# Performance work log

Measured on AMD Instinct MI355X. Metric: run time of the kernel, lower is better.

The kernel has to match this reference:

```python
import jax, jax.numpy as jnp
import numpy as np

B, T, C = 2, 1024, 2048
NH, NKV = 16, 4
HD = C // NH          # 128
NUM_REP = NH // NKV   # 4


def _apply_rotation(x, angles):
    # x: (B, T, nh, hd); angles: (T, hd//2). Equivalent to the per-pair 2x2
    # rotation matmuls in the torch code: [x0', x1'] = [[cos,-sin],[sin,cos]] @ [x0, x1]
    Bx, Tx, nh, hd = x.shape
    xp = x.reshape(Bx, Tx, nh, hd // 2, 2)
    cos = jnp.cos(angles)[None, :, None, :]  # (1, T, 1, hd//2)
    sin = jnp.sin(angles)[None, :, None, :]
    x0, x1 = xp[..., 0], xp[..., 1]
    rot = jnp.stack([cos * x0 - sin * x1, sin * x0 + cos * x1], axis=-1)
    return rot.reshape(Bx, Tx, nh, hd)


def setup_inputs() -> dict:
    key = jax.random.key(0)
    ks = jax.random.split(key, 5)
    x = jax.random.normal(ks[0], (B, T, C), dtype=jnp.float32)
    # standard RoPE angle table: pos * 10000^(-2i/hd), shape (T, hd//2)
    inv_freq = 1.0 / (10000.0 ** (jnp.arange(0, HD, 2, dtype=jnp.float32) / HD))
    angles = jnp.arange(T, dtype=jnp.float32)[:, None] * inv_freq[None, :]
    s = 0.02
    wq = jax.random.normal(ks[1], (C, C), dtype=jnp.float32) * s
    wk = jax.random.normal(ks[2], (C, NKV * HD), dtype=jnp.float32) * s
    wv = jax.random.normal(ks[3], (C, NKV * HD), dtype=jnp.float32) * s
    wo = jax.random.normal(ks[4], (C, C), dtype=jnp.float32) * s
    return {"x": x, "angles": angles, "wq": wq, "wk": wk, "wv": wv, "wo": wo}


def reference(x, angles, wq, wk, wv, wo):
    Bx, Tx, Cx = x.shape
    q = (x @ wq).reshape(Bx, Tx, NH, HD)
    k = (x @ wk).reshape(Bx, Tx, NKV, HD)
    v = (x @ wv).reshape(Bx, Tx, NKV, HD)
    q = _apply_rotation(q, angles)
    k = _apply_rotation(k, angles)
    q = q.transpose(0, 2, 1, 3)  # (B, nh, T, hd)
    k = k.transpose(0, 2, 1, 3)  # (B, nkv, T, hd)
    v = v.transpose(0, 2, 1, 3)
    if NKV != 1:
        # torch .repeat tiles kv heads: query head h uses kv head h % NKV
        k = jnp.tile(k, (1, NUM_REP, 1, 1))
        v = jnp.tile(v, (1, NUM_REP, 1, 1))
    # Faithful quirks of the source: scores = K @ Q^T (keys on rows), NO 1/sqrt(hd) scale
    scores = jnp.einsum('bhkd,bhqd->bhkq', k, q)  # (B, nh, T, T)
    mask = jnp.triu(jnp.full((Tx, Tx), -jnp.inf, dtype=scores.dtype), k=1)
    scores = scores + mask
    w = jax.nn.softmax(scores, axis=-1)
    out = jnp.einsum('bhij,bhjd->bhid', w, v)   # (B, nh, T, hd)
    out = out.transpose(0, 2, 1, 3).reshape(Bx, Tx, Cx)
    return out @ wo
```

## Files before the change

kernel.cpp:

```cpp
#include <hip/hip_runtime.h>
#include <hip/hip_bf16.h>
#include <math.h>

#define BB 2
#define TT 1024
#define CC 2048
#define NH 16
#define NKV 4
#define HD 128
#define MROWS 2048
#define QKVN 3072
#define KOFF 2048
#define VOFF 2560

typedef unsigned short u16;
typedef unsigned int   u32;
typedef _Float16 f16;
typedef _Float16 f16x8 __attribute__((ext_vector_type(8)));
typedef short    s16x8 __attribute__((ext_vector_type(8)));
typedef float    f32x4 __attribute__((ext_vector_type(4)));

__device__ __forceinline__ u16 f2h(float f) {
    union { f16 h; u16 u; } x; x.h = (f16)f; return x.u;
}
__device__ __forceinline__ float h2f(u16 u) {
    union { u16 u; f16 h; } x; x.u = u; return (float)x.h;
}

#define GLDS(gp, lp) __builtin_amdgcn_global_load_lds( \
    (const __attribute__((address_space(1))) u32*)(gp), \
    (__attribute__((address_space(3))) u32*)(lp), 16, 0, 0)

__device__ __forceinline__ void wT_tile(const float* __restrict__ src,
                                        u16* __restrict__ Wt, int Nsrc,
                                        int row_off, int idx, int t,
                                        float tile[32][33]) {
    const int k0 = (idx & 63) * 32;
    const int n0 = (idx >> 6) * 32;
    const int r = t >> 3, c4 = (t & 7) * 4;
    float4 v = *(const float4*)&src[(size_t)(k0 + r) * Nsrc + n0 + c4];
    tile[r][c4 + 0] = v.x; tile[r][c4 + 1] = v.y;
    tile[r][c4 + 2] = v.z; tile[r][c4 + 3] = v.w;
    __syncthreads();
    ushort4 o;
    o.x = f2h(tile[c4 + 0][r]); o.y = f2h(tile[c4 + 1][r]);
    o.z = f2h(tile[c4 + 2][r]); o.w = f2h(tile[c4 + 3][r]);
    *(ushort4*)&Wt[(size_t)(row_off + n0 + r) * 2048 + k0 + c4] = o;
}

__global__ __launch_bounds__(256) void prep(const float* __restrict__ x,
                                            const float* __restrict__ wq,
                                            const float* __restrict__ wk,
                                            const float* __restrict__ wv,
                                            const float* __restrict__ wo,
                                            const float* __restrict__ angles,
                                            u16* __restrict__ xb,
                                            u16* __restrict__ Wt1,
                                            u16* __restrict__ Wt2,
                                            float2* __restrict__ cs) {
    __shared__ float tile[32][33];
    const int bid = blockIdx.x, t = threadIdx.x;
    if (bid < 4096) {
        int i = bid * 256 + t;
        float4 v = ((const float4*)x)[i];
        ushort4 o;
        o.x = f2h(v.x); o.y = f2h(v.y); o.z = f2h(v.z); o.w = f2h(v.w);
        ((ushort4*)xb)[i] = o;
    } else if (bid < 8192) {
        wT_tile(wq, Wt1, 2048, 0,    bid - 4096, t, tile);
    } else if (bid < 9216) {
        wT_tile(wk, Wt1, 512,  2048, bid - 8192, t, tile);
    } else if (bid < 10240) {
        wT_tile(wv, Wt1, 512,  2560, bid - 9216, t, tile);
    } else if (bid < 14336) {
        wT_tile(wo, Wt2, 2048, 0,    bid - 10240, t, tile);
    } else {
        int i = (bid - 14336) * 256 + t;
        float a = angles[i];
        cs[i] = make_float2(cosf(a), sinf(a));
    }
}

__global__ __launch_bounds__(256) void gemm_qkv(const u16* __restrict__ A,
                                                const u16* __restrict__ Bt,
                                                u16* __restrict__ qkv,
                                                u16* __restrict__ vtg,
                                                const float2* __restrict__ cs) {
    __shared__ __align__(16) u16 As0[128 * 64];
    __shared__ __align__(16) u16 As1[128 * 64];
    __shared__ __align__(16) u16 Bs0[96 * 64];
    __shared__ __align__(16) u16 Bs1[96 * 64];
    const int t = threadIdx.x, l = t & 63, w = t >> 6;
    const int bid = blockIdx.x;
    const int xcd = bid & 7, idx = bid >> 3;
    const int bx = xcd * 4 + (idx & 3);
    const int by = idx >> 2;
    const int row0 = by * 128;
    const int col0 = bx * 96;
    const int wr = w >> 1, wc = w & 1;
    const int lg = l >> 4, ll = l & 15;
    const int K = 2048;

    f32x4 acc[4][3] = {};

#define QSTAGE(AS, BS, k0v) do {                                              \
    _Pragma("unroll")                                                         \
    for (int e_ = 0; e_ < 4; ++e_) {                                          \
        int r_ = 32 * w + 8 * e_ + (l >> 3);                                  \
        int cg_ = (l & 7) ^ (r_ & 7);                                         \
        GLDS(A + (size_t)(row0 + r_) * K + (k0v) + cg_ * 8,                   \
             (AS) + (32 * w + 8 * e_) * 64);                                  \
    }                                                                         \
    _Pragma("unroll")                                                         \
    for (int e_ = 0; e_ < 3; ++e_) {                                          \
        int r_ = 24 * w + 8 * e_ + (l >> 3);                                  \
        int cg_ = (l & 7) ^ (r_ & 7);                                         \
        GLDS(Bt + (size_t)(col0 + r_) * K + (k0v) + cg_ * 8,                  \
             (BS) + (24 * w + 8 * e_) * 64);                                  \
    }                                                                         \
} while (0)

#define QCOMP(AS, BS) do {                                                    \
    _Pragma("unroll")                                                         \
    for (int kc_ = 0; kc_ < 2; ++kc_) {                                       \
        f16x8 af_[4], bf_[3];                                                 \
        _Pragma("unroll")                                                     \
        for (int m_ = 0; m_ < 4; ++m_) {                                      \
            int row_ = wr * 64 + 16 * m_ + ll;                                \
            af_[m_] = *(const f16x8*)&(AS)[row_ * 64 +                        \
                        (((lg + 4 * kc_) ^ (ll & 7)) * 8)];                   \
        }                                                                     \
        _Pragma("unroll")                                                     \
        for (int n_ = 0; n_ < 3; ++n_) {                                      \
            int col_ = wc * 48 + 16 * n_ + ll;                                \
            bf_[n_] = *(const f16x8*)&(BS)[col_ * 64 +                        \
                        (((lg + 4 * kc_) ^ (ll & 7)) * 8)];                   \
        }                                                                     \
        _Pragma("unroll")                                                     \
        for (int m_ = 0; m_ < 4; ++m_)                                        \
            _Pragma("unroll")                                                 \
            for (int n_ = 0; n_ < 3; ++n_)                                    \
                acc[m_][n_] = __builtin_amdgcn_mfma_f32_16x16x32_f16(         \
                    af_[m_], bf_[n_], acc[m_][n_], 0, 0, 0);                  \
    }                                                                         \
} while (0)

    QSTAGE(As0, Bs0, 0);
    __syncthreads();
#pragma unroll 1
    for (int i = 0; i < 32; i += 2) {
        QSTAGE(As1, Bs1, (i + 1) * 64);
        QCOMP(As0, Bs0);
        __syncthreads();
        if (i + 2 < 32) QSTAGE(As0, Bs0, (i + 2) * 64);
        QCOMP(As1, Bs1);
        __syncthreads();
    }
#undef QSTAGE
#undef QCOMP

    const int orow = row0 + wr * 64 + lg * 4;
    const int ocol = col0 + wc * 48 + ll;
#pragma unroll
    for (int n = 0; n < 3; ++n) {
        const int col = ocol + 16 * n;
        if (col < VOFF) {
            const int p = (col & 127) >> 1;
            const bool odd = ll & 1;
#pragma unroll
            for (int m = 0; m < 4; ++m) {
#pragma unroll
                for (int r = 0; r < 4; ++r) {
                    float v = acc[m][n][r];
                    float pr = __shfl_xor(v, 1);
                    int row = orow + 16 * m + r;
                    float2 a = cs[(row & (TT - 1)) * 64 + p];
                    float res = odd ? (a.y * pr + a.x * v) : (a.x * v - a.y * pr);
                    qkv[(size_t)row * QKVN + col] = f2h(res);
                }
            }
        } else {
            int d = col - VOFF;
            const int hk = d >> 7; d &= 127;
            const int bb = orow >> 10;
            const int base_j = orow & (TT - 1);
#pragma unroll
            for (int m = 0; m < 4; ++m) {
                ushort4 pk;
                pk.x = f2h(acc[m][n][0]); pk.y = f2h(acc[m][n][1]);
                pk.z = f2h(acc[m][n][2]); pk.w = f2h(acc[m][n][3]);
                *(ushort4*)&vtg[((size_t)(bb * NKV + hk) * 128 + d) * 1024 + base_j + 16 * m] = pk;
            }
        }
    }
}

__global__ __launch_bounds__(256) void gemm_out(const u16* __restrict__ A,
                                                const u16* __restrict__ Bt,
                                                float* __restrict__ Cf) {
    __shared__ __align__(16) u16 As0[128 * 64];
    __shared__ __align__(16) u16 As1[128 * 64];
    __shared__ __align__(16) u16 Bs0[64 * 64];
    __shared__ __align__(16) u16 Bs1[64 * 64];
    const int t = threadIdx.x, l = t & 63, w = t >> 6;
    const int bid = blockIdx.x;
    const int xcd = bid & 7, idx = bid >> 3;
    const int bx = xcd * 4 + (idx & 3);
    const int by = idx >> 2;
    const int row0 = by * 128;
    const int col0 = bx * 64;
    const int wr = w >> 1, wc = w & 1;
    const int lg = l >> 4, ll = l & 15;
    const int K = 2048;

    f32x4 acc[4][2] = {};

#define GSTAGE(AS, BS, k0v) do {                                              \
    _Pragma("unroll")                                                         \
    for (int e_ = 0; e_ < 4; ++e_) {                                          \
        int r_ = 32 * w + 8 * e_ + (l >> 3);                                  \
        int cg_ = (l & 7) ^ (r_ & 7);                                         \
        GLDS(A + (size_t)(row0 + r_) * K + (k0v) + cg_ * 8,                   \
             (AS) + (32 * w + 8 * e_) * 64);                                  \
    }                                                                         \
    _Pragma("unroll")                                                         \
    for (int e_ = 0; e_ < 2; ++e_) {                                          \
        int r_ = 16 * w + 8 * e_ + (l >> 3);                                  \
        int cg_ = (l & 7) ^ (r_ & 7);                                         \
        GLDS(Bt + (size_t)(col0 + r_) * K + (k0v) + cg_ * 8,                  \
             (BS) + (16 * w + 8 * e_) * 64);                                  \
    }                                                                         \
} while (0)

#define GCOMP(AS, BS) do {                                                    \
    _Pragma("unroll")                                                         \
    for (int kc_ = 0; kc_ < 2; ++kc_) {                                       \
        f16x8 af_[4], bf_[2];                                                 \
        _Pragma("unroll")                                                     \
        for (int m_ = 0; m_ < 4; ++m_) {                                      \
            int row_ = wr * 64 + 16 * m_ + ll;                                \
            af_[m_] = *(const f16x8*)&(AS)[row_ * 64 +                        \
                        (((lg + 4 * kc_) ^ (ll & 7)) * 8)];                   \
        }                                                                     \
        _Pragma("unroll")                                                     \
        for (int n_ = 0; n_ < 2; ++n_) {                                      \
            int col_ = wc * 32 + 16 * n_ + ll;                                \
            bf_[n_] = *(const f16x8*)&(BS)[col_ * 64 +                        \
                        (((lg + 4 * kc_) ^ (ll & 7)) * 8)];                   \
        }                                                                     \
        _Pragma("unroll")                                                     \
        for (int m_ = 0; m_ < 4; ++m_)                                        \
            _Pragma("unroll")                                                 \
            for (int n_ = 0; n_ < 2; ++n_)                                    \
                acc[m_][n_] = __builtin_amdgcn_mfma_f32_16x16x32_f16(         \
                    af_[m_], bf_[n_], acc[m_][n_], 0, 0, 0);                  \
    }                                                                         \
} while (0)

    GSTAGE(As0, Bs0, 0);
    __syncthreads();
#pragma unroll 1
    for (int i = 0; i < 32; i += 2) {
        GSTAGE(As1, Bs1, (i + 1) * 64);
        GCOMP(As0, Bs0);
        __syncthreads();
        if (i + 2 < 32) GSTAGE(As0, Bs0, (i + 2) * 64);
        GCOMP(As1, Bs1);
        __syncthreads();
    }
#undef GSTAGE
#undef GCOMP

    const int orow = row0 + wr * 64 + lg * 4;
    const int ocol = col0 + wc * 32 + ll;
#pragma unroll
    for (int m = 0; m < 4; ++m)
#pragma unroll
        for (int nn = 0; nn < 2; ++nn)
#pragma unroll
            for (int r = 0; r < 4; ++r)
                Cf[(size_t)(orow + 16 * m + r) * CC + ocol + 16 * nn] =
                    acc[m][nn][r];
}

__global__ __launch_bounds__(512, 2) void attn_mfma(const u16* __restrict__ qkv,
                                                    const u16* __restrict__ vtg,
                                                    u16* __restrict__ attnb) {
    __shared__ __align__(16) u16 Qs0[64 * 128];
    __shared__ __align__(16) u16 Qs1[64 * 128];
    __shared__ __align__(16) u16 Vt0[128 * 64];
    __shared__ __align__(16) u16 Vt1[128 * 64];
    __shared__ __align__(16) u16 Ps[8 * 16 * 72];

    const int t = threadIdx.x, l = t & 63, w = t >> 6;
    const int bh = blockIdx.y;
    const int b = bh >> 4, h = bh & 15, hk = h & 3;
    const int lg = l >> 4, ll = l & 15;
    const int wl = w & 3;
    const int x = blockIdx.x;
    const int myIt = (w < 4) ? x : (15 - x);
    const int iw = myIt * 64 + wl * 16;

    const u16* qbase = qkv + (size_t)(b * TT) * QKVN + h * 128;
    const u16* vbase = vtg + (size_t)((b * NKV + hk) * 128) * 1024;

#define STAGE(j0v, Qd, Vd) do {                                               \
    _Pragma("unroll")                                                         \
    for (int e_ = 0; e_ < 2; ++e_) {                                          \
        int r_ = 4 * (2 * w + e_) + (l >> 4);                                 \
        GLDS(qbase + (size_t)((j0v) + r_) * QKVN +                            \
                 (((l & 15) ^ (r_ & 7)) * 8),                                 \
             (Qd) + 4 * (2 * w + e_) * 128);                                  \
        int d_ = 8 * (2 * w + e_) + (l >> 3);                                 \
        GLDS(vbase + (size_t)d_ * 1024 + (j0v) + (((l & 7) ^ (d_ & 7)) * 8),  \
             (Vd) + 8 * (2 * w + e_) * 64);                                   \
    }                                                                         \
} while (0)

    f16x8 kf[4];
    {
        const u16* kp = qkv + (size_t)(b * TT + iw + ll) * QKVN + KOFF + hk * 128 + lg * 8;
#pragma unroll
        for (int c = 0; c < 4; ++c) kf[c] = *(const f16x8*)(kp + 32 * c);
    }

    f32x4 o[8] = {};
    float mrun[4] = {-1e30f, -1e30f, -1e30f, -1e30f};
    float lrun[4] = {0.f, 0.f, 0.f, 0.f};

    const int nt = 16 - x;
    STAGE(0, Qs0, Vt0);
    __syncthreads();

#pragma unroll 1
    for (int jt = 0; jt < nt; ++jt) {
        u16* Qc = (jt & 1) ? Qs1 : Qs0;
        u16* Vc = (jt & 1) ? Vt1 : Vt0;
        if (jt + 1 < nt) {
            u16* Qn = (jt & 1) ? Qs0 : Qs1;
            u16* Vn = (jt & 1) ? Vt0 : Vt1;
            STAGE((jt + 1) * 64, Qn, Vn);
        }

        if (jt <= myIt) {
            f32x4 s[4] = {};
            __builtin_amdgcn_s_setprio(1);
#pragma unroll
            for (int kc = 0; kc < 4; ++kc)
#pragma unroll
                for (int n = 0; n < 4; ++n) {
                    f16x8 qf = *(const f16x8*)&Qc[(16 * n + ll) * 128 + (((lg + 4 * kc) ^ (ll & 7)) * 8)];
                    s[n] = __builtin_amdgcn_mfma_f32_16x16x32_f16(kf[kc], qf, s[n], 0, 0, 0);
                }
            __builtin_amdgcn_s_setprio(0);

            if (jt == myIt) {
#pragma unroll
                for (int n = 0; n < 4; ++n)
#pragma unroll
                    for (int r = 0; r < 4; ++r)
                        s[n][r] = (16 * n + ll <= 16 * wl + 4 * lg + r) ? s[n][r] : -1e30f;
            }

            float tml[4];
            bool need = false;
#pragma unroll
            for (int r = 0; r < 4; ++r) {
                float tm = fmaxf(fmaxf(s[0][r], s[1][r]), fmaxf(s[2][r], s[3][r]));
                tml[r] = tm;
                need |= (tm > mrun[r] + 8.0f);
            }
            if (__any(need)) {
#pragma unroll
                for (int r = 0; r < 4; ++r) {
                    float tm = tml[r];
                    tm = fmaxf(tm, __shfl_xor(tm, 1, 16));
                    tm = fmaxf(tm, __shfl_xor(tm, 2, 16));
                    tm = fmaxf(tm, __shfl_xor(tm, 4, 16));
                    tm = fmaxf(tm, __shfl_xor(tm, 8, 16));
                    float mnew = fmaxf(mrun[r], tm);
                    float al = __expf(mrun[r] - mnew);
                    lrun[r] *= al;
                    mrun[r] = mnew;
#pragma unroll
                    for (int n = 0; n < 8; ++n) o[n][r] *= al;
                }
            }
            float p[4][4];
#pragma unroll
            for (int r = 0; r < 4; ++r) {
                float ps = 0.f;
#pragma unroll
                for (int n = 0; n < 4; ++n) { p[n][r] = __expf(s[n][r] - mrun[r]); ps += p[n][r]; }
                lrun[r] += ps;
            }

            u16* pw = Ps + w * (16 * 72);
#pragma unroll
            for (int n = 0; n < 4; ++n)
#pragma unroll
                for (int r = 0; r < 4; ++r)
                    pw[(4 * lg + r) * 72 + ll + 16 * n] = f2h(p[n][r]);
            f16x8 pa0 = *(const f16x8*)&pw[ll * 72 + 8 * lg];
            f16x8 pa1 = *(const f16x8*)&pw[ll * 72 + 8 * lg + 32];

            __builtin_amdgcn_s_setprio(1);
#pragma unroll
            for (int n = 0; n < 8; ++n) {
                f16x8 vf0 = *(const f16x8*)&Vc[(16 * n + ll) * 64 + ((lg ^ (ll & 7)) * 8)];
                o[n] = __builtin_amdgcn_mfma_f32_16x16x32_f16(pa0, vf0, o[n], 0, 0, 0);
                f16x8 vf1 = *(const f16x8*)&Vc[(16 * n + ll) * 64 + (((lg + 4) ^ (ll & 7)) * 8)];
                o[n] = __builtin_amdgcn_mfma_f32_16x16x32_f16(pa1, vf1, o[n], 0, 0, 0);
            }
            __builtin_amdgcn_s_setprio(0);
        }

        __syncthreads();
    }

    u16* dst = attnb + (size_t)(b * TT + iw + 4 * lg) * CC + h * 128 + ll;
#pragma unroll
    for (int r = 0; r < 4; ++r) {
        float L = lrun[r];
        L += __shfl_xor(L, 1, 16);
        L += __shfl_xor(L, 2, 16);
        L += __shfl_xor(L, 4, 16);
        L += __shfl_xor(L, 8, 16);
        float inv = 1.0f / L;
#pragma unroll
        for (int n = 0; n < 8; ++n)
            dst[(size_t)r * CC + 16 * n] = f2h(o[n][r] * inv);
    }
#undef STAGE
}

extern "C" void kernel_launch(void* const* d_in, const int* in_sizes, int n_in,
                              void* d_out, int out_size, void* d_ws, size_t ws_size,
                              hipStream_t stream) {
    const float* x      = (const float*)d_in[0];
    const float* angles = (const float*)d_in[1];
    const float* wq     = (const float*)d_in[2];
    const float* wk     = (const float*)d_in[3];
    const float* wv     = (const float*)d_in[4];
    const float* wo     = (const float*)d_in[5];
    float* out = (float*)d_out;

    char* ws = (char*)d_ws;
    u16*    Wt1   = (u16*)ws;
    u16*    Wt2   = (u16*)(ws + 12582912);
    float2* cs    = (float2*)(ws + 20971520);
    u16*    xb    = (u16*)(ws + 21495808);
    u16*    qkvb  = (u16*)(ws + 29884416);
    u16*    vtg   = (u16*)(ws + 42467328);
    u16*    attnb = (u16*)(ws + 44564480);

    prep<<<14592, 256, 0, stream>>>(x, wq, wk, wv, wo, angles, xb, Wt1, Wt2, cs);
    gemm_qkv<<<512, 256, 0, stream>>>(xb, Wt1, qkvb, vtg, cs);
    attn_mfma<<<dim3(8, BB * NH), 512, 0, stream>>>(qkvb, vtg, attnb);
    gemm_out<<<512, 256, 0, stream>>>(attnb, Wt2, out);
}
```

Before: 112.7 us.

## Split attention key-tile range across two wave groups with split-softmax merge

Each block now handles its two query tiles sequentially, one per phase. Within each phase the causal key range is split between two 4-wave groups, each with its own double-buffered Q/V staging. The partial output, max and sum from the second group go through shared memory and are merged log-sum-exp style before writing. This is meant to shorten the per-block critical path, since before, waves 0-3 and 4-7 walked different tile counts in lockstep. The cost is more shared memory (about 146 KB), occupancy dropping to one block per CU, and an extra merge step with syncs.

```diff
diff --git a/kernel.cpp b/kernel.cpp
--- a/kernel.cpp
+++ b/kernel.cpp
@@ -283,153 +283,185 @@
                     acc[m][nn][r];
 }
 
-__global__ __launch_bounds__(512, 2) void attn_mfma(const u16* __restrict__ qkv,
+__global__ __launch_bounds__(512, 1) void attn_mfma(const u16* __restrict__ qkv,
                                                     const u16* __restrict__ vtg,
                                                     u16* __restrict__ attnb) {
-    __shared__ __align__(16) u16 Qs0[64 * 128];
-    __shared__ __align__(16) u16 Qs1[64 * 128];
-    __shared__ __align__(16) u16 Vt0[128 * 64];
-    __shared__ __align__(16) u16 Vt1[128 * 64];
-    __shared__ __align__(16) u16 Ps[8 * 16 * 72];
-
+    __shared__ __align__(16) u16 SM[74752];
     const int t = threadIdx.x, l = t & 63, w = t >> 6;
+    const int grp = w >> 2, wg = w & 3;
     const int bh = blockIdx.y;
     const int b = bh >> 4, h = bh & 15, hk = h & 3;
     const int lg = l >> 4, ll = l & 15;
-    const int wl = w & 3;
     const int x = blockIdx.x;
-    const int myIt = (w < 4) ? x : (15 - x);
-    const int iw = myIt * 64 + wl * 16;
+
+    u16* QT[2];  u16* VT[2];
+    QT[0] = SM + grp * 16384;
+    QT[1] = QT[0] + 8192;
+    VT[0] = SM + 32768 + grp * 16384;
+    VT[1] = VT[0] + 8192;
+    u16* Ps = SM + 65536;
+    float* sc = (float*)SM;
 
     const u16* qbase = qkv + (size_t)(b * TT) * QKVN + h * 128;
     const u16* vbase = vtg + (size_t)((b * NKV + hk) * 128) * 1024;
 
 #define STAGE(j0v, Qd, Vd) do {                                               \
     _Pragma("unroll")                                                         \
-    for (int e_ = 0; e_ < 2; ++e_) {                                          \
-        int r_ = 4 * (2 * w + e_) + (l >> 4);                                 \
+    for (int e_ = 0; e_ < 4; ++e_) {                                          \
+        int r_ = 16 * wg + 4 * e_ + (l >> 4);                                 \
         GLDS(qbase + (size_t)((j0v) + r_) * QKVN +                            \
                  (((l & 15) ^ (r_ & 7)) * 8),                                 \
-             (Qd) + 4 * (2 * w + e_) * 128);                                  \
-        int d_ = 8 * (2 * w + e_) + (l >> 3);                                 \
+             (Qd) + (16 * wg + 4 * e_) * 128);                                \
+        int d_ = 32 * wg + 8 * e_ + (l >> 3);                                 \
         GLDS(vbase + (size_t)d_ * 1024 + (j0v) + (((l & 7) ^ (d_ & 7)) * 8),  \
-             (Vd) + 8 * (2 * w + e_) * 64);                                   \
+             (Vd) + (32 * wg + 8 * e_) * 64);                                 \
     }                                                                         \
 } while (0)
 
-    f16x8 kf[4];
-    {
-        const u16* kp = qkv + (size_t)(b * TT + iw + ll) * QKVN + KOFF + hk * 128 + lg * 8;
-#pragma unroll
-        for (int c = 0; c < 4; ++c) kf[c] = *(const f16x8*)(kp + 32 * c);
-    }
-
-    f32x4 o[8] = {};
-    float mrun[4] = {-1e30f, -1e30f, -1e30f, -1e30f};
-    float lrun[4] = {0.f, 0.f, 0.f, 0.f};
-
-    const int nt = 16 - x;
-    STAGE(0, Qs0, Vt0);
-    __syncthreads();
-
 #pragma unroll 1
-    for (int jt = 0; jt < nt; ++jt) {
-        u16* Qc = (jt & 1) ? Qs1 : Qs0;
-        u16* Vc = (jt & 1) ? Vt1 : Vt0;
-        if (jt + 1 < nt) {
-            u16* Qn = (jt & 1) ? Qs0 : Qs1;
-            u16* Vn = (jt & 1) ? Vt0 : Vt1;
-            STAGE((jt + 1) * 64, Qn, Vn);
+    for (int ph = 0; ph < 2; ++ph) {
+        const int it = ph ? x : (15 - x);
+        const int nt = it + 1;
+        const int half = (nt + 1) >> 1;
+        const int cnt = grp ? (nt - half) : half;
+        const int jbase = grp ? half * 64 : 0;
+        const int iw = it * 64 + wg * 16;
+
+        f16x8 kf[4];
+        {
+            const u16* kp = qkv + (size_t)(b * TT + iw + ll) * QKVN + KOFF + hk * 128 + lg * 8;
+#pragma unroll
+            for (int c = 0; c < 4; ++c) kf[c] = *(const f16x8*)(kp + 32 * c);
         }
 
-        if (jt <= myIt) {
-            f32x4 s[4] = {};
-            __builtin_amdgcn_s_setprio(1);
-#pragma unroll
-            for (int kc = 0; kc < 4; ++kc)
-#pragma unroll
-                for (int n = 0; n < 4; ++n) {
-                    f16x8 qf = *(const f16x8*)&Qc[(16 * n + ll) * 128 + (((lg + 4 * kc) ^ (ll & 7)) * 8)];
-                    s[n] = __builtin_amdgcn_mfma_f32_16x16x32_f16(kf[kc], qf, s[n], 0, 0, 0);
-                }
-            __builtin_amdgcn_s_setprio(0);
-
-            if (jt == myIt) {
+        f32x4 o[8] = {};
+        float mrun[4] = {-1e30f, -1e30f, -1e30f, -1e30f};
+        float lrun[4] = {0.f, 0.f, 0.f, 0.f};
+
+        if (cnt > 0) STAGE(jbase, QT[0], VT[0]);
+        __syncthreads();
+
+#pragma unroll 1
+        for (int r = 0; r < half; ++r) {
+            u16* Qc = QT[r & 1];
+            u16* Vc = VT[r & 1];
+            if (r + 1 < cnt) STAGE(jbase + (r + 1) * 64, QT[(r + 1) & 1], VT[(r + 1) & 1]);
+
+            if (r < cnt) {
+                const int jt = (grp ? half : 0) + r;
+                f32x4 s[4] = {};
+                __builtin_amdgcn_s_setprio(1);
+#pragma unroll
+                for (int kc = 0; kc < 4; ++kc)
+#pragma unroll
+                    for (int n = 0; n < 4; ++n) {
+                        f16x8 qf = *(const f16x8*)&Qc[(16 * n + ll) * 128 + (((lg + 4 * kc) ^ (ll & 7)) * 8)];
+                        s[n] = __builtin_amdgcn_mfma_f32_16x16x32_f16(kf[kc], qf, s[n], 0, 0, 0);
+                    }
+                __builtin_amdgcn_s_setprio(0);
+
+                if (jt == it) {
+#pragma unroll
+                    for (int n = 0; n < 4; ++n)
+#pragma unroll
+                        for (int rr = 0; rr < 4; ++rr)
+                            s[n][rr] = (16 * n + ll <= 16 * wg + 4 * lg + rr) ? s[n][rr] : -1e30f;
+                }
+
+                float tml[4];
+                bool need = false;
+#pragma unroll
+                for (int rr = 0; rr < 4; ++rr) {
+                    float tm = fmaxf(fmaxf(s[0][rr], s[1][rr]), fmaxf(s[2][rr], s[3][rr]));
+                    tml[rr] = tm;
+                    need |= (tm > mrun[rr] + 8.0f);
+                }
+                if (__any(need)) {
+#pragma unroll
+                    for (int rr = 0; rr < 4; ++rr) {
+                        float tm = tml[rr];
+                        tm = fmaxf(tm, __shfl_xor(tm, 1, 16));
+                        tm = fmaxf(tm, __shfl_xor(tm, 2, 16));
+                        tm = fmaxf(tm, __shfl_xor(tm, 4, 16));
+                        tm = fmaxf(tm, __shfl_xor(tm, 8, 16));
+                        float mnew = fmaxf(mrun[rr], tm);
+                        float al = __expf(mrun[rr] - mnew);
+                        lrun[rr] *= al;
+                        mrun[rr] = mnew;
+#pragma unroll
+                        for (int n = 0; n < 8; ++n) o[n][rr] *= al;
+                    }
+                }
+                float p[4][4];
+#pragma unroll
+                for (int rr = 0; rr < 4; ++rr) {
+                    float ps = 0.f;
+#pragma unroll
+                    for (int n = 0; n < 4; ++n) { p[n][rr] = __expf(s[n][rr] - mrun[rr]); ps += p[n][rr]; }
+                    lrun[rr] += ps;
+                }
+
+                u16* pw = Ps + w * (16 * 72);
 #pragma unroll
                 for (int n = 0; n < 4; ++n)
 #pragma unroll
-                    for (int r = 0; r < 4; ++r)
-                        s[n][r] = (16 * n + ll <= 16 * wl + 4 * lg + r) ? s[n][r] : -1e30f;
+                    for (int rr = 0; rr < 4; ++rr)
+                        pw[(4 * lg + rr) * 72 + ll + 16 * n] = f2h(p[n][rr]);
+                f16x8 pa0 = *(const f16x8*)&pw[ll * 72 + 8 * lg];
+                f16x8 pa1 = *(const f16x8*)&pw[ll * 72 + 8 * lg + 32];
+
+                __builtin_amdgcn_s_setprio(1);
+#pragma unroll
+                for (int n = 0; n < 8; ++n) {
+                    f16x8 vf0 = *(const f16x8*)&Vc[(16 * n + ll) * 64 + ((lg ^ (ll & 7)) * 8)];
+                    o[n] = __builtin_amdgcn_mfma_f32_16x16x32_f16(pa0, vf0, o[n], 0, 0, 0);
+                    f16x8 vf1 = *(const f16x8*)&Vc[(16 * n + ll) * 64 + (((lg + 4) ^ (ll & 7)) * 8)];
+                    o[n] = __builtin_amdgcn_mfma_f32_16x16x32_f16(pa1, vf1, o[n], 0, 0, 0);
+                }
+                __builtin_amdgcn_s_setprio(0);
             }
 
-            float tml[4];
-            bool need = false;
-#pragma unroll
-            for (int r = 0; r < 4; ++r) {
-                float tm = fmaxf(fmaxf(s[0][r], s[1][r]), fmaxf(s[2][r], s[3][r]));
-                tml[r] = tm;
-                need |= (tm > mrun[r] + 8.0f);
+            __syncthreads();
+        }
+
+        if (grp == 1) {
+            const int base = (wg * 64 + l) * 40;
+#pragma unroll
+            for (int n = 0; n < 8; ++n)
+#pragma unroll
+                for (int rr = 0; rr < 4; ++rr)
+                    sc[base + n * 4 + rr] = o[n][rr];
+#pragma unroll
+            for (int rr = 0; rr < 4; ++rr) {
+                sc[base + 32 + rr] = mrun[rr];
+                sc[base + 36 + rr] = lrun[rr];
             }
-            if (__any(need)) {
-#pragma unroll
-                for (int r = 0; r < 4; ++r) {
-                    float tm = tml[r];
-                    tm = fmaxf(tm, __shfl_xor(tm, 1, 16));
-                    tm = fmaxf(tm, __shfl_xor(tm, 2, 16));
-                    tm = fmaxf(tm, __shfl_xor(tm, 4, 16));
-                    tm = fmaxf(tm, __shfl_xor(tm, 8, 16));
-                    float mnew = fmaxf(mrun[r], tm);
-                    float al = __expf(mrun[r] - mnew);
-                    lrun[r] *= al;
-                    mrun[r] = mnew;
-#pragma unroll
-                    for (int n = 0; n < 8; ++n) o[n][r] *= al;
+        }
+        __syncthreads();
+        if (grp == 0) {
+            const int base = (wg * 64 + l) * 40;
+            u16* dst = attnb + (size_t)(b * TT + iw + 4 * lg) * CC + h * 128 + ll;
+#pragma unroll
+            for (int rr = 0; rr < 4; ++rr) {
+                float mB = sc[base + 32 + rr];
+                float lB = sc[base + 36 + rr];
+                float m  = fmaxf(mrun[rr], mB);
+                float aA = __expf(mrun[rr] - m);
+                float aB = __expf(mB - m);
+                float L = lrun[rr] * aA + lB * aB;
+                L += __shfl_xor(L, 1, 16);
+                L += __shfl_xor(L, 2, 16);
+                L += __shfl_xor(L, 4, 16);
+                L += __shfl_xor(L, 8, 16);
+                float inv = 1.0f / L;
+#pragma unroll
+                for (int n = 0; n < 8; ++n) {
+                    float oo = o[n][rr] * aA + sc[base + n * 4 + rr] * aB;
+                    dst[(size_t)rr * CC + 16 * n] = f2h(oo * inv);
                 }
             }
-            float p[4][4];
-#pragma unroll
-            for (int r = 0; r < 4; ++r) {
-                float ps = 0.f;
-#pragma unroll
-                for (int n = 0; n < 4; ++n) { p[n][r] = __expf(s[n][r] - mrun[r]); ps += p[n][r]; }
-                lrun[r] += ps;
-            }
-
-            u16* pw = Ps + w * (16 * 72);
-#pragma unroll
-            for (int n = 0; n < 4; ++n)
-#pragma unroll
-                for (int r = 0; r < 4; ++r)
-                    pw[(4 * lg + r) * 72 + ll + 16 * n] = f2h(p[n][r]);
-            f16x8 pa0 = *(const f16x8*)&pw[ll * 72 + 8 * lg];
-            f16x8 pa1 = *(const f16x8*)&pw[ll * 72 + 8 * lg + 32];
-
-            __builtin_amdgcn_s_setprio(1);
-#pragma unroll
-            for (int n = 0; n < 8; ++n) {
-                f16x8 vf0 = *(const f16x8*)&Vc[(16 * n + ll) * 64 + ((lg ^ (ll & 7)) * 8)];
-                o[n] = __builtin_amdgcn_mfma_f32_16x16x32_f16(pa0, vf0, o[n], 0, 0, 0);
-                f16x8 vf1 = *(const f16x8*)&Vc[(16 * n + ll) * 64 + (((lg + 4) ^ (ll & 7)) * 8)];
-                o[n] = __builtin_amdgcn_mfma_f32_16x16x32_f16(pa1, vf1, o[n], 0, 0, 0);
-            }
-            __builtin_amdgcn_s_setprio(0);
         }
-
-        __syncthreads();
-    }
-
-    u16* dst = attnb + (size_t)(b * TT + iw + 4 * lg) * CC + h * 128 + ll;
-#pragma unroll
-    for (int r = 0; r < 4; ++r) {
-        float L = lrun[r];
-        L += __shfl_xor(L, 1, 16);
-        L += __shfl_xor(L, 2, 16);
-        L += __shfl_xor(L, 4, 16);
-        L += __shfl_xor(L, 8, 16);
-        float inv = 1.0f / L;
-#pragma unroll
-        for (int n = 0; n < 8; ++n)
-            dst[(size_t)r * CC + 16 * n] = f2h(o[n][r] * inv);
+        __syncthreads();
     }
 #undef STAGE
 }
```

After: 117.7 us. 4.4% more time.
